# Optimization experiments

Measured on AMD Instinct MI355X. Metric: run time of the kernel, lower is better.

Reference implementation:

```python
import jax, jax.numpy as jnp
import numpy as np

IN_F = 1024
OUT_F = 1024
DEGREE = 7  # degree+1 = 8 Chebyshev terms


def setup_inputs() -> dict:
    key = jax.random.key(0)
    k1, k2, k3 = jax.random.split(key, 3)
    x = jax.random.normal(k1, (16384, IN_F), dtype=jnp.float32)
    std = 1.0 / (IN_F * (DEGREE + 1))
    cheby_coeffs = jax.random.normal(k2, (OUT_F, IN_F, DEGREE + 1), dtype=jnp.float32) * std
    # xavier_uniform for base_weight [out, in]
    limit = float(np.sqrt(6.0 / (IN_F + OUT_F)))
    base_weight = jax.random.uniform(k3, (OUT_F, IN_F), dtype=jnp.float32, minval=-limit, maxval=limit)
    return {"x": x, "cheby_coeffs": cheby_coeffs, "base_weight": base_weight}


def _cheby_basis(x_norm, degree):
    terms = [jnp.ones_like(x_norm), x_norm]
    for _ in range(2, degree + 1):
        terms.append(2.0 * x_norm * terms[-1] - terms[-2])
    return jnp.stack(terms, axis=-1)  # [b, i, d+1]


def reference(x, cheby_coeffs, base_weight):
    x_norm = jnp.tanh(x)
    basis = _cheby_basis(x_norm, DEGREE)               # [b, i, d]
    kan_out = jnp.einsum('bid,oid->bo', basis, cheby_coeffs)
    base_out = x @ base_weight.T                        # F.linear
    return kan_out + base_out
```

## Files before the change

### kernel.cpp

```cpp
#include <hip/hip_runtime.h>
#include <hip/hip_bf16.h>
#include <stdint.h>

typedef short short8 __attribute__((ext_vector_type(8)));
typedef float f32x4 __attribute__((ext_vector_type(4)));

#define BATCH 16384
#define INF 1024
#define OUTF 1024
#define KD 8192

__device__ __forceinline__ unsigned short bfb(float f) {
    __hip_bfloat16 h = __float2bfloat16(f);
    return __builtin_bit_cast(unsigned short, h);
}

__global__ void prep_w(const float* __restrict__ C, const float* __restrict__ W,
                       unsigned short* __restrict__ Bw) {
    int g = blockIdx.x * 256 + threadIdx.x;
    int o = g >> 10, i = g & 1023;
    const float* src = C + ((size_t)o * 8192 + i * 8);
    float4 v0 = *(const float4*)src;
    float4 v1 = *(const float4*)(src + 4);
    v0.x = W[o * 1024 + i];
    short8 r;
    r[0] = bfb(v0.x); r[1] = bfb(v0.y); r[2] = bfb(v0.z); r[3] = bfb(v0.w);
    r[4] = bfb(v1.x); r[5] = bfb(v1.y); r[6] = bfb(v1.z); r[7] = bfb(v1.w);
    *(short8*)(Bw + (size_t)g * 8) = r;
}

__global__ void prep_bias(const float* __restrict__ C, float* __restrict__ bias) {
    int o = blockIdx.x;
    int tid = threadIdx.x;
    float s = 0.f;
    for (int i = tid; i < 1024; i += 256)
        s += C[(size_t)o * 8192 + (size_t)i * 8];
    #pragma unroll
    for (int off = 32; off > 0; off >>= 1) s += __shfl_down(s, off);
    __shared__ float red[4];
    if ((tid & 63) == 0) red[tid >> 6] = s;
    __syncthreads();
    if (tid == 0) bias[o] = red[0] + red[1] + red[2] + red[3];
}

__global__ __launch_bounds__(256, 2)
void cheby_gemm(const float* __restrict__ X, const unsigned short* __restrict__ Bw,
                const float* __restrict__ bias, float* __restrict__ Out) {
    __shared__ unsigned short As[128][72];
    __shared__ unsigned short Bs[128][72];

    const int tid  = threadIdx.x;
    const int lane = tid & 63;
    const int wave = tid >> 6;
    const int wm = (wave >> 1) * 64;
    const int wn = (wave & 1) * 64;

    const int bid = blockIdx.x;
    const int m0 = (bid >> 3) * 128;
    const int n0 = (bid & 7) * 128;

    const int lr = lane & 15;
    const int lg = lane >> 4;

    f32x4 acc[4][4] = {};

    for (int k0 = 0; k0 < KD; k0 += 64) {
        const int i0 = k0 >> 3;
        __syncthreads();
        #pragma unroll
        for (int j = 0; j < 4; ++j) {
            int p = tid + 256 * j;
            int row = p >> 3, f = p & 7;
            float xv = X[(size_t)(m0 + row) * INF + i0 + f];
            float e  = __builtin_amdgcn_exp2f(xv * 2.8853900817779268f);
            float xn = 1.0f - 2.0f * __builtin_amdgcn_rcpf(1.0f + e);
            float x2 = xn + xn;
            float t2 = x2 * xn - 1.0f;
            float t3 = x2 * t2 - xn;
            float t4 = x2 * t3 - t2;
            float t5 = x2 * t4 - t3;
            float t6 = x2 * t5 - t4;
            float t7 = x2 * t6 - t5;
            short8 v;
            v[0] = bfb(xv); v[1] = bfb(xn); v[2] = bfb(t2); v[3] = bfb(t3);
            v[4] = bfb(t4); v[5] = bfb(t5); v[6] = bfb(t6); v[7] = bfb(t7);
            *(short8*)&As[row][f * 8] = v;
        }
        #pragma unroll
        for (int j = 0; j < 4; ++j) {
            int p = tid + 256 * j;
            int r = p >> 3, c = p & 7;
            short8 v = *(const short8*)(Bw + (size_t)(n0 + r) * KD + k0 + c * 8);
            *(short8*)&Bs[r][c * 8] = v;
        }
        __syncthreads();
        #pragma unroll
        for (int kk = 0; kk < 2; ++kk) {
            short8 af[4], bfr[4];
            #pragma unroll
            for (int mi = 0; mi < 4; ++mi)
                af[mi] = *(const short8*)&As[wm + mi * 16 + lr][kk * 32 + lg * 8];
            #pragma unroll
            for (int ni = 0; ni < 4; ++ni)
                bfr[ni] = *(const short8*)&Bs[wn + ni * 16 + lr][kk * 32 + lg * 8];
            #pragma unroll
            for (int mi = 0; mi < 4; ++mi) {
                #pragma unroll
                for (int ni = 0; ni < 4; ++ni) {
                    acc[mi][ni] = __builtin_amdgcn_mfma_f32_16x16x32_bf16(
                        af[mi], bfr[ni], acc[mi][ni], 0, 0, 0);
                }
            }
        }
    }

    #pragma unroll
    for (int mi = 0; mi < 4; ++mi) {
        #pragma unroll
        for (int ni = 0; ni < 4; ++ni) {
            int col = n0 + wn + ni * 16 + lr;
            float bv = bias[col];
            #pragma unroll
            for (int r = 0; r < 4; ++r) {
                int row = m0 + wm + mi * 16 + lg * 4 + r;
                Out[(size_t)row * OUTF + col] = acc[mi][ni][r] + bv;
            }
        }
    }
}

extern "C" void kernel_launch(void* const* d_in, const int* in_sizes, int n_in,
                              void* d_out, int out_size, void* d_ws, size_t ws_size,
                              hipStream_t stream) {
    const float* x = (const float*)d_in[0];
    const float* C = (const float*)d_in[1];
    const float* W = (const float*)d_in[2];
    float* out = (float*)d_out;

    unsigned short* Bw = (unsigned short*)d_ws;
    float* bias = (float*)((char*)d_ws + (size_t)16 * 1024 * 1024);

    prep_w<<<4096, 256, 0, stream>>>(C, W, Bw);
    prep_bias<<<1024, 256, 0, stream>>>(C, bias);
    cheby_gemm<<<1024, 256, 0, stream>>>(x, Bw, bias, out);
}
```

Baseline: 322.4 us.

## Rewrite Chebyshev GEMM with 256x256 tiles, LDS double buffering and direct global-to-LDS loads

The GEMM kernel is restructured into 256x256 output tiles computed by 512 threads, with double-buffered LDS for both operands. B tiles are loaded straight into LDS with global_load_lds, and X loads are prefetched two tiles ahead so the Chebyshev basis expansion overlaps the MFMA work. LDS rows use an XOR swizzle in place of padding to avoid bank conflicts, and the block index is remapped for better L2 reuse. The code relies on hand-placed barriers, waitcnts and setprio, which makes it fragile and raises register pressure (32 accumulators per thread).

Result: faster. 263.2 us (-18.4%).

```diff
diff --git a/kernel.cpp b/kernel.cpp
--- a/kernel.cpp
+++ b/kernel.cpp
@@ -5,10 +5,8 @@
 typedef short short8 __attribute__((ext_vector_type(8)));
 typedef float f32x4 __attribute__((ext_vector_type(4)));
 
-#define BATCH 16384
-#define INF 1024
-#define OUTF 1024
 #define KD 8192
+#define NT 128
 
 __device__ __forceinline__ unsigned short bfb(float f) {
     __hip_bfloat16 h = __float2bfloat16(f);
@@ -43,87 +41,170 @@
     if (tid == 0) bias[o] = red[0] + red[1] + red[2] + red[3];
 }
 
-__global__ __launch_bounds__(256, 2)
+
+#define GLDS(NXT_, C_, TT_) \
+    __builtin_amdgcn_global_load_lds( \
+        (const __attribute__((address_space(1))) unsigned int*)((const char*)Bw + boff[C_] + (size_t)(TT_) * 128), \
+        (__attribute__((address_space(3))) unsigned int*)(&Bs[NXT_][(wave * 4 + (C_)) * 8][0]), 16, 0, 0)
+
+#define LDA8(DST_, CUR_, MI_, KK_) { \
+    int row_ = wm + (MI_) * 16 + lr; \
+    DST_ = *(const short8*)((const char*)&As[CUR_][0][0] + row_ * 128 + ((((KK_) * 4 + lg) ^ (row_ & 7)) * 16)); }
+
+#define LDB8(DST_, CUR_, NI_, KK_) { \
+    int row_ = wn + (NI_) * 16 + lr; \
+    DST_ = *(const short8*)((const char*)&Bs[CUR_][0][0] + row_ * 128 + ((((KK_) * 4 + lg) ^ (row_ & 7)) * 16)); }
+
+#define XLOAD(DST_, TI_) { \
+    const float* ap_ = xbase + (size_t)(TI_) * 8; \
+    asm volatile("global_load_dwordx4 %0, %1, off" : "=&v"(DST_) : "v"(ap_)); }
+
+#define XFORM(NXT_, XV_) { \
+    _Pragma("unroll") \
+    for (int j_ = 0; j_ < 4; ++j_) { \
+        float xv_ = XV_[j_]; \
+        float e_  = __builtin_amdgcn_exp2f(xv_ * 2.8853900817779268f); \
+        float xn_ = 1.0f - 2.0f * __builtin_amdgcn_rcpf(1.0f + e_); \
+        float x2_ = xn_ + xn_; \
+        float t2_ = x2_ * xn_ - 1.0f; \
+        float t3_ = x2_ * t2_ - xn_; \
+        float t4_ = x2_ * t3_ - t2_; \
+        float t5_ = x2_ * t4_ - t3_; \
+        float t6_ = x2_ * t5_ - t4_; \
+        float t7_ = x2_ * t6_ - t5_; \
+        short8 v_; \
+        v_[0] = bfb(xv_); v_[1] = bfb(xn_); v_[2] = bfb(t2_); v_[3] = bfb(t3_); \
+        v_[4] = bfb(t4_); v_[5] = bfb(t5_); v_[6] = bfb(t6_); v_[7] = bfb(t7_); \
+        *(short8*)((char*)&As[NXT_][0][0] + woff[j_]) = v_; \
+    } }
+
+#define MFMA16(MB_) { \
+    acc[MB_+0][0] = __builtin_amdgcn_mfma_f32_16x16x32_bf16(a0_, b0_, acc[MB_+0][0], 0, 0, 0); \
+    acc[MB_+0][1] = __builtin_amdgcn_mfma_f32_16x16x32_bf16(a0_, b1_, acc[MB_+0][1], 0, 0, 0); \
+    acc[MB_+0][2] = __builtin_amdgcn_mfma_f32_16x16x32_bf16(a0_, b2_, acc[MB_+0][2], 0, 0, 0); \
+    acc[MB_+0][3] = __builtin_amdgcn_mfma_f32_16x16x32_bf16(a0_, b3_, acc[MB_+0][3], 0, 0, 0); \
+    acc[MB_+1][0] = __builtin_amdgcn_mfma_f32_16x16x32_bf16(a1_, b0_, acc[MB_+1][0], 0, 0, 0); \
+    acc[MB_+1][1] = __builtin_amdgcn_mfma_f32_16x16x32_bf16(a1_, b1_, acc[MB_+1][1], 0, 0, 0); \
+    acc[MB_+1][2] = __builtin_amdgcn_mfma_f32_16x16x32_bf16(a1_, b2_, acc[MB_+1][2], 0, 0, 0); \
+    acc[MB_+1][3] = __builtin_amdgcn_mfma_f32_16x16x32_bf16(a1_, b3_, acc[MB_+1][3], 0, 0, 0); \
+    acc[MB_+2][0] = __builtin_amdgcn_mfma_f32_16x16x32_bf16(a2_, b0_, acc[MB_+2][0], 0, 0, 0); \
+    acc[MB_+2][1] = __builtin_amdgcn_mfma_f32_16x16x32_bf16(a2_, b1_, acc[MB_+2][1], 0, 0, 0); \
+    acc[MB_+2][2] = __builtin_amdgcn_mfma_f32_16x16x32_bf16(a2_, b2_, acc[MB_+2][2], 0, 0, 0); \
+    acc[MB_+2][3] = __builtin_amdgcn_mfma_f32_16x16x32_bf16(a2_, b3_, acc[MB_+2][3], 0, 0, 0); \
+    acc[MB_+3][0] = __builtin_amdgcn_mfma_f32_16x16x32_bf16(a3_, b0_, acc[MB_+3][0], 0, 0, 0); \
+    acc[MB_+3][1] = __builtin_amdgcn_mfma_f32_16x16x32_bf16(a3_, b1_, acc[MB_+3][1], 0, 0, 0); \
+    acc[MB_+3][2] = __builtin_amdgcn_mfma_f32_16x16x32_bf16(a3_, b2_, acc[MB_+3][2], 0, 0, 0); \
+    acc[MB_+3][3] = __builtin_amdgcn_mfma_f32_16x16x32_bf16(a3_, b3_, acc[MB_+3][3], 0, 0, 0); }
+
+#define TILE(CUR_, NXT_, T_, XC_, XD_) { \
+    const int tn_ = ((T_) + 1 < NT) ? (T_) + 1 : NT - 1; \
+    const int tl_ = ((T_) + 2 < NT) ? (T_) + 2 : NT - 1; \
+    short8 a0_, a1_, a2_, a3_, b0_, b1_, b2_, b3_; \
+     \
+    LDA8(a0_, CUR_, 0, 0) LDA8(a1_, CUR_, 1, 0) LDA8(a2_, CUR_, 2, 0) LDA8(a3_, CUR_, 3, 0) \
+    LDB8(b0_, CUR_, 0, 0) LDB8(b1_, CUR_, 1, 0) LDB8(b2_, CUR_, 2, 0) LDB8(b3_, CUR_, 3, 0) \
+    GLDS(NXT_, 0, tn_); GLDS(NXT_, 1, tn_); \
+    __builtin_amdgcn_s_barrier(); \
+    __builtin_amdgcn_s_setprio(1); \
+    MFMA16(0) \
+    __builtin_amdgcn_s_setprio(0); \
+    __builtin_amdgcn_s_barrier(); \
+     \
+    LDA8(a0_, CUR_, 4, 0) LDA8(a1_, CUR_, 5, 0) LDA8(a2_, CUR_, 6, 0) LDA8(a3_, CUR_, 7, 0) \
+    GLDS(NXT_, 2, tn_); GLDS(NXT_, 3, tn_); \
+    asm volatile("s_waitcnt vmcnt(4)" ::: "memory"); \
+    __builtin_amdgcn_sched_barrier(0); \
+    XFORM(NXT_, XC_) \
+    __builtin_amdgcn_s_barrier(); \
+    __builtin_amdgcn_s_setprio(1); \
+    MFMA16(4) \
+    __builtin_amdgcn_s_setprio(0); \
+    __builtin_amdgcn_s_barrier(); \
+     \
+    LDA8(a0_, CUR_, 0, 1) LDA8(a1_, CUR_, 1, 1) LDA8(a2_, CUR_, 2, 1) LDA8(a3_, CUR_, 3, 1) \
+    LDB8(b0_, CUR_, 0, 1) LDB8(b1_, CUR_, 1, 1) LDB8(b2_, CUR_, 2, 1) LDB8(b3_, CUR_, 3, 1) \
+    XLOAD(XD_, tl_) \
+    __builtin_amdgcn_s_barrier(); \
+    __builtin_amdgcn_s_setprio(1); \
+    MFMA16(0) \
+    __builtin_amdgcn_s_setprio(0); \
+    __builtin_amdgcn_s_barrier(); \
+     \
+    LDA8(a0_, CUR_, 4, 1) LDA8(a1_, CUR_, 5, 1) LDA8(a2_, CUR_, 6, 1) LDA8(a3_, CUR_, 7, 1) \
+    __builtin_amdgcn_s_barrier(); \
+    __builtin_amdgcn_s_setprio(1); \
+    MFMA16(4) \
+    __builtin_amdgcn_s_setprio(0); \
+    asm volatile("s_waitcnt vmcnt(1) lgkmcnt(0)" ::: "memory"); \
+    __builtin_amdgcn_sched_barrier(0); \
+    __builtin_amdgcn_s_barrier(); \
+    __builtin_amdgcn_sched_barrier(0); \
+}
+
+__global__ __launch_bounds__(512, 2)
 void cheby_gemm(const float* __restrict__ X, const unsigned short* __restrict__ Bw,
                 const float* __restrict__ bias, float* __restrict__ Out) {
-    __shared__ unsigned short As[128][72];
-    __shared__ unsigned short Bs[128][72];
+    __shared__ unsigned short As[2][256][64];
+    __shared__ unsigned short Bs[2][256][64];
 
     const int tid  = threadIdx.x;
     const int lane = tid & 63;
     const int wave = tid >> 6;
-    const int wm = (wave >> 1) * 64;
-    const int wn = (wave & 1) * 64;
-
-    const int bid = blockIdx.x;
-    const int m0 = (bid >> 3) * 128;
-    const int n0 = (bid & 7) * 128;
-
+
+    int bid = blockIdx.x;
+    int lin = (bid & 7) * 32 + (bid >> 3);
+    const int m0 = (lin & 63) << 8;
+    const int n0 = (lin >> 6) << 8;
+
+    const int wm = (wave >> 2) * 128;
+    const int wn = (wave & 3) * 64;
     const int lr = lane & 15;
     const int lg = lane >> 4;
 
-    f32x4 acc[4][4] = {};
-
-    for (int k0 = 0; k0 < KD; k0 += 64) {
-        const int i0 = k0 >> 3;
-        __syncthreads();
+    const int arow = tid >> 1;
+    const int af0  = (tid & 1) * 4;
+    const float* xbase = X + (size_t)(m0 + arow) * 1024 + af0;
+    unsigned int woff[4];
+    #pragma unroll
+    for (int j = 0; j < 4; ++j)
+        woff[j] = (unsigned)(arow * 128 + (((af0 + j) ^ (arow & 7)) * 16));
+
+    unsigned int boff[4];
+    #pragma unroll
+    for (int c = 0; c < 4; ++c) {
+        int row   = (wave * 4 + c) * 8 + (lane >> 3);
+        int chunk = (lane & 7) ^ (lane >> 3);
+        boff[c] = ((unsigned)(n0 + row) * 8192u + (unsigned)chunk * 8u) * 2u;
+    }
+
+    f32x4 acc[8][4] = {};
+    f32x4 xA, xB;
+
+    GLDS(0, 0, 0); GLDS(0, 1, 0); GLDS(0, 2, 0); GLDS(0, 3, 0);
+    XLOAD(xA, 0)
+    XLOAD(xB, 1)
+    asm volatile("s_waitcnt vmcnt(1)" ::: "memory");
+    __builtin_amdgcn_sched_barrier(0);
+    XFORM(0, xA)
+    asm volatile("s_waitcnt lgkmcnt(0)" ::: "memory");
+    __builtin_amdgcn_s_barrier();
+    __builtin_amdgcn_sched_barrier(0);
+
+    for (int t = 0; t < NT; t += 2) {
+        TILE(0, 1, t,     xB, xA)
+        TILE(1, 0, t + 1, xA, xB)
+    }
+
+    #pragma unroll
+    for (int ni = 0; ni < 4; ++ni) {
+        int col = n0 + wn + ni * 16 + lr;
+        float bv = bias[col];
         #pragma unroll
-        for (int j = 0; j < 4; ++j) {
-            int p = tid + 256 * j;
-            int row = p >> 3, f = p & 7;
-            float xv = X[(size_t)(m0 + row) * INF + i0 + f];
-            float e  = __builtin_amdgcn_exp2f(xv * 2.8853900817779268f);
-            float xn = 1.0f - 2.0f * __builtin_amdgcn_rcpf(1.0f + e);
-            float x2 = xn + xn;
-            float t2 = x2 * xn - 1.0f;
-            float t3 = x2 * t2 - xn;
-            float t4 = x2 * t3 - t2;
-            float t5 = x2 * t4 - t3;
-            float t6 = x2 * t5 - t4;
-            float t7 = x2 * t6 - t5;
-            short8 v;
-            v[0] = bfb(xv); v[1] = bfb(xn); v[2] = bfb(t2); v[3] = bfb(t3);
-            v[4] = bfb(t4); v[5] = bfb(t5); v[6] = bfb(t6); v[7] = bfb(t7);
-            *(short8*)&As[row][f * 8] = v;
-        }
-        #pragma unroll
-        for (int j = 0; j < 4; ++j) {
-            int p = tid + 256 * j;
-            int r = p >> 3, c = p & 7;
-            short8 v = *(const short8*)(Bw + (size_t)(n0 + r) * KD + k0 + c * 8);
-            *(short8*)&Bs[r][c * 8] = v;
-        }
-        __syncthreads();
-        #pragma unroll
-        for (int kk = 0; kk < 2; ++kk) {
-            short8 af[4], bfr[4];
-            #pragma unroll
-            for (int mi = 0; mi < 4; ++mi)
-                af[mi] = *(const short8*)&As[wm + mi * 16 + lr][kk * 32 + lg * 8];
-            #pragma unroll
-            for (int ni = 0; ni < 4; ++ni)
-                bfr[ni] = *(const short8*)&Bs[wn + ni * 16 + lr][kk * 32 + lg * 8];
-            #pragma unroll
-            for (int mi = 0; mi < 4; ++mi) {
-                #pragma unroll
-                for (int ni = 0; ni < 4; ++ni) {
-                    acc[mi][ni] = __builtin_amdgcn_mfma_f32_16x16x32_bf16(
-                        af[mi], bfr[ni], acc[mi][ni], 0, 0, 0);
-                }
-            }
-        }
-    }
-
-    #pragma unroll
-    for (int mi = 0; mi < 4; ++mi) {
-        #pragma unroll
-        for (int ni = 0; ni < 4; ++ni) {
-            int col = n0 + wn + ni * 16 + lr;
-            float bv = bias[col];
+        for (int mi = 0; mi < 8; ++mi) {
             #pragma unroll
             for (int r = 0; r < 4; ++r) {
                 int row = m0 + wm + mi * 16 + lg * 4 + r;
-                Out[(size_t)row * OUTF + col] = acc[mi][ni][r] + bv;
+                Out[(size_t)row * 1024 + col] = acc[mi][ni][r] + bv;
             }
         }
     }
@@ -142,5 +223,5 @@
 
     prep_w<<<4096, 256, 0, stream>>>(C, W, Bw);
     prep_bias<<<1024, 256, 0, stream>>>(C, bias);
-    cheby_gemm<<<1024, 256, 0, stream>>>(x, Bw, bias, out);
-}
+    cheby_gemm<<<256, 512, 0, stream>>>(x, Bw, bias, out);
+}
```

## Rewrite Chebyshev GEMM with 256x256 tiles, 32x32 MFMA, double-buffered async loads

Applied to the files above, without the earlier changes.

Replaces the main GEMM kernel with a 512-thread, 256x256-tile version that uses 32x32x16 bf16 MFMA and double-buffered LDS. Weight tiles stream straight into swizzled LDS through global_load_lds. Raw x values are staged in LDS, and the Chebyshev basis is computed in registers right before each MFMA instead of being written to LDS as bf16. Block indices are remapped for L2 locality and MFMA sections get raised priority. The aim is to cut LDS traffic and per-tile sync stalls and to overlap global loads with compute. In exchange each basis value is recomputed once per wave column group (4x redundant ALU), and register pressure is high.

Result: no change. 321.0 us (-0.4%).

```diff
diff --git a/kernel.cpp b/kernel.cpp
--- a/kernel.cpp
+++ b/kernel.cpp
@@ -3,16 +3,30 @@
 #include <stdint.h>
 
 typedef short short8 __attribute__((ext_vector_type(8)));
-typedef float f32x4 __attribute__((ext_vector_type(4)));
+typedef float f32x16 __attribute__((ext_vector_type(16)));
 
-#define BATCH 16384
-#define INF 1024
-#define OUTF 1024
 #define KD 8192
+#define NT 128
 
 __device__ __forceinline__ unsigned short bfb(float f) {
     __hip_bfloat16 h = __float2bfloat16(f);
     return __builtin_bit_cast(unsigned short, h);
+}
+
+__device__ __forceinline__ short8 cheby8(float xv) {
+    float e  = __builtin_amdgcn_exp2f(xv * 2.8853900817779268f);
+    float xn = 1.0f - 2.0f * __builtin_amdgcn_rcpf(1.0f + e);
+    float x2 = xn + xn;
+    float t2 = x2 * xn - 1.0f;
+    float t3 = x2 * t2 - xn;
+    float t4 = x2 * t3 - t2;
+    float t5 = x2 * t4 - t3;
+    float t6 = x2 * t5 - t4;
+    float t7 = x2 * t6 - t5;
+    short8 v;
+    v[0] = bfb(xv); v[1] = bfb(xn); v[2] = bfb(t2); v[3] = bfb(t3);
+    v[4] = bfb(t4); v[5] = bfb(t5); v[6] = bfb(t6); v[7] = bfb(t7);
+    return v;
 }
 
 __global__ void prep_w(const float* __restrict__ C, const float* __restrict__ W,
@@ -43,87 +57,111 @@
     if (tid == 0) bias[o] = red[0] + red[1] + red[2] + red[3];
 }
 
-__global__ __launch_bounds__(256, 2)
+
+#define GLDS(NXT_, C_, TT_) \
+    __builtin_amdgcn_global_load_lds( \
+        (const __attribute__((address_space(1))) unsigned int*)((const char*)Bw + boff[C_] + (size_t)(TT_) * 128), \
+        (__attribute__((address_space(3))) unsigned int*)(&Bs[NXT_][(wave * 4 + (C_)) * 8][0]), 16, 0, 0)
+
+#define PHASE(CUR_, KK_) { \
+    const int fb_ = (KK_) * 2 + lg;   \
+    float xv0_ = Xs[CUR_][fb_][wm + lr]; \
+    float xv1_ = Xs[CUR_][fb_][wm + 32 + lr]; \
+    float xv2_ = Xs[CUR_][fb_][wm + 64 + lr]; \
+    float xv3_ = Xs[CUR_][fb_][wm + 96 + lr]; \
+    const int row0_ = wn + lr, row1_ = wn + 32 + lr; \
+    short8 b0_ = *(const short8*)((const char*)&Bs[CUR_][0][0] + row0_ * 128 + ((fb_ ^ (row0_ & 7)) * 16)); \
+    short8 b1_ = *(const short8*)((const char*)&Bs[CUR_][0][0] + row1_ * 128 + ((fb_ ^ (row1_ & 7)) * 16)); \
+    short8 a0_ = cheby8(xv0_); \
+    short8 a1_ = cheby8(xv1_); \
+    short8 a2_ = cheby8(xv2_); \
+    short8 a3_ = cheby8(xv3_); \
+    __builtin_amdgcn_s_setprio(1); \
+    acc[0][0] = __builtin_amdgcn_mfma_f32_32x32x16_bf16(a0_, b0_, acc[0][0], 0, 0, 0); \
+    acc[0][1] = __builtin_amdgcn_mfma_f32_32x32x16_bf16(a0_, b1_, acc[0][1], 0, 0, 0); \
+    acc[1][0] = __builtin_amdgcn_mfma_f32_32x32x16_bf16(a1_, b0_, acc[1][0], 0, 0, 0); \
+    acc[1][1] = __builtin_amdgcn_mfma_f32_32x32x16_bf16(a1_, b1_, acc[1][1], 0, 0, 0); \
+    acc[2][0] = __builtin_amdgcn_mfma_f32_32x32x16_bf16(a2_, b0_, acc[2][0], 0, 0, 0); \
+    acc[2][1] = __builtin_amdgcn_mfma_f32_32x32x16_bf16(a2_, b1_, acc[2][1], 0, 0, 0); \
+    acc[3][0] = __builtin_amdgcn_mfma_f32_32x32x16_bf16(a3_, b0_, acc[3][0], 0, 0, 0); \
+    acc[3][1] = __builtin_amdgcn_mfma_f32_32x32x16_bf16(a3_, b1_, acc[3][1], 0, 0, 0); \
+    __builtin_amdgcn_s_setprio(0); \
+}
+
+#define TILE(CUR_, NXT_, T_) { \
+    const int tn_ = ((T_) + 1 < NT) ? (T_) + 1 : NT - 1; \
+    float4 xr_ = *(const float4*)(xbase + (size_t)tn_ * 8);   \
+    GLDS(NXT_, 0, tn_); GLDS(NXT_, 1, tn_); GLDS(NXT_, 2, tn_); GLDS(NXT_, 3, tn_); \
+    PHASE(CUR_, 0) \
+    PHASE(CUR_, 1) \
+    Xs[NXT_][xf + 0][arow] = xr_.x; \
+    Xs[NXT_][xf + 1][arow] = xr_.y; \
+    Xs[NXT_][xf + 2][arow] = xr_.z; \
+    Xs[NXT_][xf + 3][arow] = xr_.w; \
+    PHASE(CUR_, 2) \
+    PHASE(CUR_, 3) \
+    __syncthreads(); \
+}
+
+__global__ __launch_bounds__(512, 2)
 void cheby_gemm(const float* __restrict__ X, const unsigned short* __restrict__ Bw,
                 const float* __restrict__ bias, float* __restrict__ Out) {
-    __shared__ unsigned short As[128][72];
-    __shared__ unsigned short Bs[128][72];
+    __shared__ unsigned short Bs[2][256][64];
+    __shared__ float Xs[2][8][256];
 
     const int tid  = threadIdx.x;
     const int lane = tid & 63;
     const int wave = tid >> 6;
-    const int wm = (wave >> 1) * 64;
-    const int wn = (wave & 1) * 64;
 
-    const int bid = blockIdx.x;
-    const int m0 = (bid >> 3) * 128;
-    const int n0 = (bid & 7) * 128;
+    int bid = blockIdx.x;
+    int lin = (bid & 7) * 32 + (bid >> 3);
+    const int m0 = (lin & 63) << 8;
+    const int n0 = (lin >> 6) << 8;
 
-    const int lr = lane & 15;
-    const int lg = lane >> 4;
+    const int wm = (wave >> 2) * 128;
+    const int wn = (wave & 3) * 64;
+    const int lr = lane & 31;
+    const int lg = lane >> 5;
 
-    f32x4 acc[4][4] = {};
+    const int arow = tid >> 1;
+    const int xf   = (tid & 1) * 4;
+    const float* xbase = X + (size_t)(m0 + arow) * 1024 + xf;
 
-    for (int k0 = 0; k0 < KD; k0 += 64) {
-        const int i0 = k0 >> 3;
+    unsigned int boff[4];
+    #pragma unroll
+    for (int c = 0; c < 4; ++c) {
+        int row   = (wave * 4 + c) * 8 + (lane >> 3);
+        int chunk = (lane & 7) ^ (lane >> 3);
+        boff[c] = ((unsigned)(n0 + row) * 8192u + (unsigned)chunk * 8u) * 2u;
+    }
+
+    f32x16 acc[4][2] = {};
+
+    {
+        float4 xr_ = *(const float4*)(xbase);
+        GLDS(0, 0, 0); GLDS(0, 1, 0); GLDS(0, 2, 0); GLDS(0, 3, 0);
+        Xs[0][xf + 0][arow] = xr_.x;
+        Xs[0][xf + 1][arow] = xr_.y;
+        Xs[0][xf + 2][arow] = xr_.z;
+        Xs[0][xf + 3][arow] = xr_.w;
         __syncthreads();
-        #pragma unroll
-        for (int j = 0; j < 4; ++j) {
-            int p = tid + 256 * j;
-            int row = p >> 3, f = p & 7;
-            float xv = X[(size_t)(m0 + row) * INF + i0 + f];
-            float e  = __builtin_amdgcn_exp2f(xv * 2.8853900817779268f);
-            float xn = 1.0f - 2.0f * __builtin_amdgcn_rcpf(1.0f + e);
-            float x2 = xn + xn;
-            float t2 = x2 * xn - 1.0f;
-            float t3 = x2 * t2 - xn;
-            float t4 = x2 * t3 - t2;
-            float t5 = x2 * t4 - t3;
-            float t6 = x2 * t5 - t4;
-            float t7 = x2 * t6 - t5;
-            short8 v;
-            v[0] = bfb(xv); v[1] = bfb(xn); v[2] = bfb(t2); v[3] = bfb(t3);
-            v[4] = bfb(t4); v[5] = bfb(t5); v[6] = bfb(t6); v[7] = bfb(t7);
-            *(short8*)&As[row][f * 8] = v;
-        }
-        #pragma unroll
-        for (int j = 0; j < 4; ++j) {
-            int p = tid + 256 * j;
-            int r = p >> 3, c = p & 7;
-            short8 v = *(const short8*)(Bw + (size_t)(n0 + r) * KD + k0 + c * 8);
-            *(short8*)&Bs[r][c * 8] = v;
-        }
-        __syncthreads();
-        #pragma unroll
-        for (int kk = 0; kk < 2; ++kk) {
-            short8 af[4], bfr[4];
-            #pragma unroll
-            for (int mi = 0; mi < 4; ++mi)
-                af[mi] = *(const short8*)&As[wm + mi * 16 + lr][kk * 32 + lg * 8];
-            #pragma unroll
-            for (int ni = 0; ni < 4; ++ni)
-                bfr[ni] = *(const short8*)&Bs[wn + ni * 16 + lr][kk * 32 + lg * 8];
-            #pragma unroll
-            for (int mi = 0; mi < 4; ++mi) {
-                #pragma unroll
-                for (int ni = 0; ni < 4; ++ni) {
-                    acc[mi][ni] = __builtin_amdgcn_mfma_f32_16x16x32_bf16(
-                        af[mi], bfr[ni], acc[mi][ni], 0, 0, 0);
-                }
-            }
-        }
+    }
+
+    for (int t = 0; t < NT; t += 2) {
+        TILE(0, 1, t)
+        TILE(1, 0, t + 1)
     }
 
     #pragma unroll
-    for (int mi = 0; mi < 4; ++mi) {
+    for (int ni = 0; ni < 2; ++ni) {
+        int col = n0 + wn + ni * 32 + lr;
+        float bv = bias[col];
         #pragma unroll
-        for (int ni = 0; ni < 4; ++ni) {
-            int col = n0 + wn + ni * 16 + lr;
-            float bv = bias[col];
+        for (int mi = 0; mi < 4; ++mi) {
             #pragma unroll
-            for (int r = 0; r < 4; ++r) {
-                int row = m0 + wm + mi * 16 + lg * 4 + r;
-                Out[(size_t)row * OUTF + col] = acc[mi][ni][r] + bv;
+            for (int r = 0; r < 16; ++r) {
+                int row = m0 + wm + mi * 32 + 4 * lg + (r & 3) + 8 * (r >> 2);
+                Out[(size_t)row * 1024 + col] = acc[mi][ni][r] + bv;
             }
         }
     }
@@ -142,5 +180,5 @@
 
     prep_w<<<4096, 256, 0, stream>>>(C, W, Bw);
     prep_bias<<<1024, 256, 0, stream>>>(C, bias);
-    cheby_gemm<<<1024, 256, 0, stream>>>(x, Bw, bias, out);
+    cheby_gemm<<<256, 512, 0, stream>>>(x, Bw, bias, out);
 }
```
